# Kernel tuning notes

Measured on AMD Instinct MI355X. Metric: run time of the kernel, lower is better.

Reference implementation:

```python
import jax, jax.numpy as jnp
import numpy as np
from jax import lax

B, CIN, COUT, H, W = 4, 256, 256, 64, 64
KH = KW = 3
STRIDE = PAD = DIL = 1
GROUPS = 1
K = KH * KW
HO = (H + 2 * PAD - DIL * (KH - 1) - 1) // STRIDE + 1
WO = (W + 2 * PAD - DIL * (KW - 1) - 1) // STRIDE + 1
DN = ('NCHW', 'OIHW', 'NCHW')


def _sep_conv(x, dw, pw):
    # Separable2d: depthwise kxk conv (stride/pad/dilation) then pointwise 1x1.
    y = lax.conv_general_dilated(x, dw, (STRIDE, STRIDE), [(PAD, PAD), (PAD, PAD)],
                                 rhs_dilation=(DIL, DIL), feature_group_count=x.shape[1],
                                 dimension_numbers=DN)
    return lax.conv_general_dilated(y, pw, (1, 1), 'VALID', dimension_numbers=DN)


def _deform_conv2d(x, offset, mask, weight, bias):
    Bb, Cin, Hh, Ww = x.shape
    O = weight.shape[0]
    G = offset.shape[1] // (2 * K)  # offset groups
    offs = offset.reshape(Bb, G, K, 2, HO, WO)
    dy, dx = offs[:, :, :, 0], offs[:, :, :, 1]  # [B,G,K,Ho,Wo]
    ki, kj = jnp.meshgrid(jnp.arange(KH), jnp.arange(KW), indexing='ij')
    base_y = (-PAD + ki.reshape(K, 1) * DIL + jnp.arange(HO)[None, :] * STRIDE).astype(x.dtype)  # [K,Ho]
    base_x = (-PAD + kj.reshape(K, 1) * DIL + jnp.arange(WO)[None, :] * STRIDE).astype(x.dtype)  # [K,Wo]
    py = base_y[None, None, :, :, None] + dy  # [B,G,K,Ho,Wo]
    px = base_x[None, None, :, None, :] + dx

    xg = x.reshape(Bb, G, Cin // G, Hh, Ww)

    def bilinear(img, py, px):
        # img [C,H,W], py/px [K,Ho,Wo]; zero-padding outside bounds.
        y0 = jnp.floor(py)
        x0 = jnp.floor(px)
        out = jnp.zeros((img.shape[0],) + py.shape, img.dtype)
        for a, (iy, wy) in enumerate((((y0), (y0 + 1 - py)), ((y0 + 1), (py - y0)))):
            for b, (ix, wx) in enumerate((((x0), (x0 + 1 - px)), ((x0 + 1), (px - x0)))):
                valid = (iy >= 0) & (iy < Hh) & (ix >= 0) & (ix < Ww)
                iyc = jnp.clip(iy, 0, Hh - 1).astype(jnp.int32)
                ixc = jnp.clip(ix, 0, Ww - 1).astype(jnp.int32)
                v = img[:, iyc, ixc]  # [C,K,Ho,Wo]
                out = out + v * (wy * wx * valid)[None]
        return out

    sampled = jax.vmap(jax.vmap(bilinear))(xg, py, px)  # [B,G,C/G,K,Ho,Wo]
    m = mask.reshape(Bb, G, K, HO, WO)
    sampled = sampled * m[:, :, None]

    cols = sampled.reshape(Bb, Cin, K, HO, WO).reshape(Bb, GROUPS, Cin // GROUPS, K, HO, WO)
    wr = weight.reshape(GROUPS, O // GROUPS, Cin // GROUPS, K)
    out = jnp.einsum('bgckhw,gock->bgohw', cols, wr).reshape(Bb, O, HO, WO)
    return out + bias[None, :, None, None]


def setup_inputs() -> dict:
    key = jax.random.key(0)
    ks = jax.random.split(key, 7)
    x = jax.random.normal(ks[0], (B, CIN, H, W), jnp.float32)
    weight = jax.random.normal(ks[1], (COUT, CIN // GROUPS, KH, KW), jnp.float32) / np.sqrt(CIN * K)
    bias = jax.random.normal(ks[2], (COUT,), jnp.float32) * 0.01
    off_dw = jax.random.normal(ks[3], (CIN, 1, KH, KW), jnp.float32) * 0.01
    off_pw = jax.random.normal(ks[4], (2 * K * GROUPS, CIN, 1, 1), jnp.float32) * 0.01
    mask_dw = jax.random.normal(ks[5], (CIN, 1, KH, KW), jnp.float32) * 0.01
    mask_pw = jax.random.normal(ks[6], (K * GROUPS, CIN, 1, 1), jnp.float32) * 0.01
    return dict(x=x, weight=weight, bias=bias, off_dw=off_dw, off_pw=off_pw,
                mask_dw=mask_dw, mask_pw=mask_pw)


def reference(x, weight, bias, off_dw, off_pw, mask_dw, mask_pw):
    offset = _sep_conv(x, off_dw, off_pw)                       # [B,2*K,Ho,Wo]
    mask = jax.nn.sigmoid(_sep_conv(x, mask_dw, mask_pw)) * 2.0  # MaskSigmoid(scale=2)
    return _deform_conv2d(x, offset, mask, weight, bias)
```

## Files before the change

### kernel.cpp

```cpp
#include <hip/hip_runtime.h>

#define CIN   256
#define COUT  256
#define HH    64
#define WW    64
#define KD    2304
#define NPIX  16384
#define SPLIT 16
#define CPS   (CIN / SPLIT)

typedef __attribute__((ext_vector_type(8))) short  short8v;
typedef __attribute__((ext_vector_type(4))) float  float4v;
typedef __attribute__((ext_vector_type(4))) unsigned short ushort4v;
typedef __attribute__((ext_vector_type(2))) unsigned int uint2v;
typedef unsigned int u32;
typedef unsigned short u16;

__device__ __forceinline__ u16 f2bf(float f) {
  union { float f; unsigned u; } v; v.f = f;
  unsigned r = v.u + 0x7FFFu + ((v.u >> 16) & 1u);
  return (u16)(r >> 16);
}
__device__ __forceinline__ float bf2f(u16 h) {
  union { unsigned u; float f; } v; v.u = ((unsigned)h) << 16;
  return v.f;
}

__device__ __forceinline__ void gload_lds16(const void* g, void* l) {
  __builtin_amdgcn_global_load_lds((const __attribute__((address_space(1))) u32*)g,
                                   (__attribute__((address_space(3))) u32*)l, 16, 0, 0);
}

__global__ __launch_bounds__(256) void offmask_part_kernel(
    const float* __restrict__ x,
    const float* __restrict__ off_dw, const float* __restrict__ off_pw,
    const float* __restrict__ mask_dw, const float* __restrict__ mask_pw,
    float* __restrict__ part)
{
  int m = blockIdx.x * 256 + threadIdx.x;
  int s = blockIdx.y;
  int b = m >> 12, pix = m & 4095;
  int ho = pix >> 6, wo = pix & 63;
  const float* xb = x + (size_t)b * CIN * 4096;

  float acc[27];
#pragma unroll
  for (int j = 0; j < 27; ++j) acc[j] = 0.f;

  int c0 = s * CPS;
  for (int ci = 0; ci < CPS; ++ci) {
    int c = c0 + ci;
    const float* xc = xb + (size_t)c * 4096;
    float d_off = 0.f, d_msk = 0.f;
#pragma unroll
    for (int t = 0; t < 9; ++t) {
      int gy = ho + t / 3 - 1, gx = wo + t % 3 - 1;
      bool ok = (gy >= 0) & (gy < HH) & (gx >= 0) & (gx < WW);
      float v = ok ? xc[gy * 64 + gx] : 0.f;
      d_off += v * off_dw[c * 9 + t];
      d_msk += v * mask_dw[c * 9 + t];
    }
#pragma unroll
    for (int j = 0; j < 18; ++j) acc[j] += d_off * off_pw[j * 256 + c];
#pragma unroll
    for (int j = 0; j < 9; ++j) acc[18 + j] += d_msk * mask_pw[j * 256 + c];
  }
  float* pp = part + ((size_t)s * NPIX + m) * 32;
#pragma unroll
  for (int j = 0; j < 27; ++j) pp[j] = acc[j];
}

__global__ __launch_bounds__(256) void offmask_reduce_kernel(
    const float* __restrict__ part, float* __restrict__ rec)
{
  int i = blockIdx.x * 256 + threadIdx.x;
  int m = i >> 5, j = i & 31;
  if (j >= 27) { rec[i] = 0.f; return; }
  float sum = 0.f;
#pragma unroll
  for (int s = 0; s < SPLIT; ++s) sum += part[((size_t)s * NPIX + m) * 32 + j];
  rec[i] = (j < 18) ? sum : 2.f / (1.f + __expf(-sum));
}

__global__ __launch_bounds__(256) void wconv_kernel(const float* __restrict__ w,
                                                    u16* __restrict__ wb)
{
  int i = blockIdx.x * 256 + threadIdx.x;
  int co = i / KD, rem = i - co * KD;
  int c = rem / 9, kk = rem - c * 9;
  wb[co * KD + kk * 256 + c] = f2bf(w[i]);
}

__global__ __launch_bounds__(256) void xpose_kernel(const float* __restrict__ x,
                                                    u16* __restrict__ xt)
{
  __shared__ float t[64][65];
  int ptile = blockIdx.x;
  int ctile = blockIdx.y;
  int b     = blockIdx.z;
  int tid = threadIdx.x;
  const float* xb = x + (size_t)b * CIN * 4096 + (size_t)ctile * 64 * 4096 + ptile * 64;
#pragma unroll
  for (int i = 0; i < 16; ++i) {
    int c = i * 4 + (tid >> 6), p = tid & 63;
    t[c][p] = xb[(size_t)c * 4096 + p];
  }
  __syncthreads();
  u16* xo = xt + ((size_t)b * 4096 + ptile * 64) * 256 + ctile * 64;
#pragma unroll
  for (int i = 0; i < 16; ++i) {
    int p = i * 4 + (tid >> 6), c = tid & 63;
    xo[(size_t)p * 256 + c] = f2bf(t[c][p]);
  }
}

__global__ __launch_bounds__(512) void gemm_fused_kernel(
    const u16* __restrict__ A,
    const u16* __restrict__ xt,
    const float* __restrict__ rec,
    const float* __restrict__ bias,
    float* __restrict__ out,
    float* __restrict__ tmp)
{
  __shared__ __align__(16) u16 lA[2][256 * 32];
  __shared__ __align__(16) u16 lB[2][64 * 32];
  const int tid = threadIdx.x;
  const int bid = blockIdx.x;
  const int h   = bid & 1;
  const int ptile = bid >> 1;
  const int m0  = ptile * 64;
  const int b_img = ptile >> 6;
  const int cbase = h * 128;
  const int wave = tid >> 6, lane = tid & 63;
  const int wm = wave >> 1, wn = wave & 1;
  const int rl = lane & 15, kq = lane >> 4;
  const int sA = (kq ^ (rl & 3) ^ ((rl >> 2) & 3)) * 8;

  const int rA  = tid >> 2;
  const int koA = ((tid & 3) ^ (rA & 3) ^ ((rA >> 2) & 3)) * 8;
  const u16* aRow0 = A + (size_t)rA * KD + koA;
  const u16* aRow1 = A + (size_t)(rA + 128) * KD + koA;

  const int spx = tid >> 3;
  const int sc4 = (tid & 7) * 4;
  const int m_px = m0 + spx;
  const int ho = (m_px & 4095) >> 6, wo = m_px & 63;
  const float* rp = rec + (size_t)m_px * 32;
  const u16* xb = xt + (size_t)b_img * 4096 * 256;
  const int wAddr = spx * 32 +
                    ((((tid >> 1) & 3) ^ ((spx & 3) ^ ((spx >> 2) & 3))) * 8) +
                    (tid & 1) * 4;

  u32 cOff[4];
  float cW[4];

#define KCOL(t_) (((t_) >> 2) * 256 + cbase + ((t_) & 3) * 32)

#define CALC_CORNERS(kk_) do {                                             \
    float dy = rp[(kk_) * 2], dx = rp[(kk_) * 2 + 1], msk = rp[18 + (kk_)];\
    float py  = (float)(ho - 1 + ((kk_) / 3)) + dy;                        \
    float pxf = (float)(wo - 1 + ((kk_) % 3)) + dx;                        \
    float fy = floorf(py), fx = floorf(pxf);                               \
    int y0 = (int)fy, x0 = (int)fx;                                        \
    float wy1 = py - fy, wy0 = 1.f - wy1;                                  \
    float wx1 = pxf - fx, wx0 = 1.f - wx1;                                 \
    _Pragma("unroll")                                                      \
    for (int cr = 0; cr < 4; ++cr) {                                       \
      int iy = y0 + (cr >> 1), ix = x0 + (cr & 1);                         \
      bool valid = (iy >= 0) & (iy < HH) & (ix >= 0) & (ix < WW);          \
      int iyc = min(max(iy, 0), HH - 1), ixc = min(max(ix, 0), WW - 1);    \
      cOff[cr] = (u32)(iyc * 64 + ixc) * 256;                              \
      float wy = (cr >> 1) ? wy1 : wy0;                                    \
      float wx = (cr & 1) ? wx1 : wx0;                                     \
      cW[cr] = valid ? (wy * wx * msk) : 0.f;                              \
    }                                                                      \
  } while (0)

#define STAGE_A(t, bufi) do {                                              \
    int k0_ = KCOL(t);                                                     \
    gload_lds16(aRow0 + k0_, lA[bufi] + tid * 8);                          \
    gload_lds16(aRow1 + k0_, lA[bufi] + (tid + 512) * 8);                  \
  } while (0)

  float4v acc[4][2];
#pragma unroll
  for (int m = 0; m < 4; ++m)
#pragma unroll
    for (int n = 0; n < 2; ++n) acc[m][n] = float4v{0.f, 0.f, 0.f, 0.f};

  {
    CALC_CORNERS(0);
    int c0n = cbase + sc4;
    ushort4v v0 = *(const ushort4v*)(xb + cOff[0] + c0n);
    ushort4v v1 = *(const ushort4v*)(xb + cOff[1] + c0n);
    ushort4v v2 = *(const ushort4v*)(xb + cOff[2] + c0n);
    ushort4v v3 = *(const ushort4v*)(xb + cOff[3] + c0n);
    float a0 = cW[0]*bf2f(v0[0]) + cW[1]*bf2f(v1[0]) + cW[2]*bf2f(v2[0]) + cW[3]*bf2f(v3[0]);
    float a1 = cW[0]*bf2f(v0[1]) + cW[1]*bf2f(v1[1]) + cW[2]*bf2f(v2[1]) + cW[3]*bf2f(v3[1]);
    float a2 = cW[0]*bf2f(v0[2]) + cW[1]*bf2f(v1[2]) + cW[2]*bf2f(v2[2]) + cW[3]*bf2f(v3[2]);
    float a3 = cW[0]*bf2f(v0[3]) + cW[1]*bf2f(v1[3]) + cW[2]*bf2f(v2[3]) + cW[3]*bf2f(v3[3]);
    uint2v wv;
    wv[0] = (u32)f2bf(a0) | ((u32)f2bf(a1) << 16);
    wv[1] = (u32)f2bf(a2) | ((u32)f2bf(a3) << 16);
    *(uint2v*)&lB[0][wAddr] = wv;
    STAGE_A(0, 0);
  }
  __syncthreads();

#pragma unroll 4
  for (int ks = 0; ks < 36; ++ks) {
    const int cur = ks & 1;
    ushort4v v0, v1, v2, v3;
    const bool have = (ks < 35);
    if (have) {
      STAGE_A(ks + 1, cur ^ 1);
      int ksn = ks + 1;
      if ((ksn & 3) == 0) CALC_CORNERS(ksn >> 2);
      int c0n = cbase + (ksn & 3) * 32 + sc4;
      v0 = *(const ushort4v*)(xb + cOff[0] + c0n);
      v1 = *(const ushort4v*)(xb + cOff[1] + c0n);
      v2 = *(const ushort4v*)(xb + cOff[2] + c0n);
      v3 = *(const ushort4v*)(xb + cOff[3] + c0n);
    }
    short8v af[4], bf[2];
#pragma unroll
    for (int m = 0; m < 4; ++m)
      af[m] = *(const short8v*)&lA[cur][(wm * 64 + m * 16 + rl) * 32 + sA];
#pragma unroll
    for (int n = 0; n < 2; ++n)
      bf[n] = *(const short8v*)&lB[cur][(wn * 32 + n * 16 + rl) * 32 + sA];
#pragma unroll
    for (int m = 0; m < 4; ++m)
#pragma unroll
      for (int n = 0; n < 2; ++n)
        acc[m][n] = __builtin_amdgcn_mfma_f32_16x16x32_bf16(af[m], bf[n], acc[m][n], 0, 0, 0);
    if (have) {
      float a0 = cW[0]*bf2f(v0[0]) + cW[1]*bf2f(v1[0]) + cW[2]*bf2f(v2[0]) + cW[3]*bf2f(v3[0]);
      float a1 = cW[0]*bf2f(v0[1]) + cW[1]*bf2f(v1[1]) + cW[2]*bf2f(v2[1]) + cW[3]*bf2f(v3[1]);
      float a2 = cW[0]*bf2f(v0[2]) + cW[1]*bf2f(v1[2]) + cW[2]*bf2f(v2[2]) + cW[3]*bf2f(v3[2]);
      float a3 = cW[0]*bf2f(v0[3]) + cW[1]*bf2f(v1[3]) + cW[2]*bf2f(v2[3]) + cW[3]*bf2f(v3[3]);
      uint2v wv;
      wv[0] = (u32)f2bf(a0) | ((u32)f2bf(a1) << 16);
      wv[1] = (u32)f2bf(a2) | ((u32)f2bf(a3) << 16);
      *(uint2v*)&lB[cur ^ 1][wAddr] = wv;
    }
    __syncthreads();
  }
#undef STAGE_A
#undef CALC_CORNERS
#undef KCOL

  const int p_base = (m0 & 4095) + wn * 32;
  float* db = (h ? tmp : out) + (size_t)b_img * COUT * 4096;
#pragma unroll
  for (int m = 0; m < 4; ++m) {
#pragma unroll
    for (int j = 0; j < 4; ++j) {
      int co = wm * 64 + m * 16 + kq * 4 + j;
      float bv = h ? 0.f : bias[co];
#pragma unroll
      for (int n = 0; n < 2; ++n) {
        int pp = p_base + n * 16 + rl;
        db[(size_t)co * 4096 + pp] = acc[m][n][j] + bv;
      }
    }
  }
}

__global__ __launch_bounds__(256) void add_kernel(float* __restrict__ out,
                                                  const float* __restrict__ tmp)
{
  int i = blockIdx.x * 256 + threadIdx.x;
  float4v a = *(const float4v*)(out + (size_t)i * 4);
  float4v b = *(const float4v*)(tmp + (size_t)i * 4);
  a += b;
  *(float4v*)(out + (size_t)i * 4) = a;
}

extern "C" void kernel_launch(void* const* d_in, const int* in_sizes, int n_in,
                              void* d_out, int out_size, void* d_ws, size_t ws_size,
                              hipStream_t stream) {
  const float* x       = (const float*)d_in[0];
  const float* weight  = (const float*)d_in[1];
  const float* bias    = (const float*)d_in[2];
  const float* off_dw  = (const float*)d_in[3];
  const float* off_pw  = (const float*)d_in[4];
  const float* mask_dw = (const float*)d_in[5];
  const float* mask_pw = (const float*)d_in[6];

  if (ws_size < 45219840ull) return;
  float* rec  = (float*)d_ws;
  u16*   wb   = (u16*)((char*)d_ws + 2097152);
  u16*   xt   = (u16*)((char*)d_ws + 3276800);
  float* part = (float*)((char*)d_ws + 11665408);
  float* tmp  = part;
  float* out  = (float*)d_out;

  wconv_kernel<<<dim3(2304), dim3(256), 0, stream>>>(weight, wb);
  offmask_part_kernel<<<dim3(NPIX / 256, SPLIT), dim3(256), 0, stream>>>(
      x, off_dw, off_pw, mask_dw, mask_pw, part);
  offmask_reduce_kernel<<<dim3(NPIX * 32 / 256), dim3(256), 0, stream>>>(part, rec);
  xpose_kernel<<<dim3(64, 4, 4), dim3(256), 0, stream>>>(x, xt);
  gemm_fused_kernel<<<dim3(512), dim3(512), 0, stream>>>(wb, xt, rec, bias, out, tmp);
  add_kernel<<<dim3((COUT * NPIX / 4) / 256), dim3(256), 0, stream>>>(out, tmp);
}
```

Measured before the change: 106.5 us.

## Switch to fp16 packed bilinear blend and split-K into four channel quarters

Weights and transposed activations are now stored as fp16 instead of bf16. The bilinear blend uses packed half2 multiply-adds, and the GEMM uses the f16 MFMA instead of the bf16 one. The GEMM grid doubles from 512 to 1024 blocks by splitting the channel reduction into four 64-channel quarters, which should improve occupancy across CUs and shorten each block's K loop. The cost is three partial output buffers plus a heavier final add kernel that reads them, and fp16 overflow and precision risk in the blend and inputs.

Result: slower. 110.8 us (+4.0%).

```diff
diff --git a/kernel.cpp b/kernel.cpp
--- a/kernel.cpp
+++ b/kernel.cpp
@@ -11,20 +11,15 @@
 
 typedef __attribute__((ext_vector_type(8))) short  short8v;
 typedef __attribute__((ext_vector_type(4))) float  float4v;
-typedef __attribute__((ext_vector_type(4))) unsigned short ushort4v;
 typedef __attribute__((ext_vector_type(2))) unsigned int uint2v;
+typedef _Float16 h2 __attribute__((ext_vector_type(2)));
+typedef _Float16 h8 __attribute__((ext_vector_type(8)));
 typedef unsigned int u32;
 typedef unsigned short u16;
 
-__device__ __forceinline__ u16 f2bf(float f) {
-  union { float f; unsigned u; } v; v.f = f;
-  unsigned r = v.u + 0x7FFFu + ((v.u >> 16) & 1u);
-  return (u16)(r >> 16);
-}
-__device__ __forceinline__ float bf2f(u16 h) {
-  union { unsigned u; float f; } v; v.u = ((unsigned)h) << 16;
-  return v.f;
-}
+__device__ __forceinline__ h2 as_h2(u32 v) { union { u32 u; h2 h; } x; x.u = v; return x.h; }
+__device__ __forceinline__ u32 as_u32(h2 h) { union { u32 u; h2 h; } x; x.h = h; return x.u; }
+__device__ __forceinline__ u16 f2h_bits(float f) { _Float16 h = (_Float16)f; return *(u16*)&h; }
 
 __device__ __forceinline__ void gload_lds16(const void* g, void* l) {
   __builtin_amdgcn_global_load_lds((const __attribute__((address_space(1))) u32*)g,
@@ -88,7 +83,7 @@
   int i = blockIdx.x * 256 + threadIdx.x;
   int co = i / KD, rem = i - co * KD;
   int c = rem / 9, kk = rem - c * 9;
-  wb[co * KD + kk * 256 + c] = f2bf(w[i]);
+  wb[co * KD + kk * 256 + c] = f2h_bits(w[i]);
 }
 
 __global__ __launch_bounds__(256) void xpose_kernel(const float* __restrict__ x,
@@ -110,7 +105,7 @@
 #pragma unroll
   for (int i = 0; i < 16; ++i) {
     int p = i * 4 + (tid >> 6), c = tid & 63;
-    xo[(size_t)p * 256 + c] = f2bf(t[c][p]);
+    xo[(size_t)p * 256 + c] = f2h_bits(t[c][p]);
   }
 }
 
@@ -126,11 +121,11 @@
   __shared__ __align__(16) u16 lB[2][64 * 32];
   const int tid = threadIdx.x;
   const int bid = blockIdx.x;
-  const int h   = bid & 1;
-  const int ptile = bid >> 1;
+  const int h   = bid & 3;
+  const int ptile = bid >> 2;
   const int m0  = ptile * 64;
   const int b_img = ptile >> 6;
-  const int cbase = h * 128;
+  const int cbase = h * 64;
   const int wave = tid >> 6, lane = tid & 63;
   const int wm = wave >> 1, wn = wave & 1;
   const int rl = lane & 15, kq = lane >> 4;
@@ -152,9 +147,9 @@
                     (tid & 1) * 4;
 
   u32 cOff[4];
-  float cW[4];
-
-#define KCOL(t_) (((t_) >> 2) * 256 + cbase + ((t_) & 3) * 32)
+  h2  wh[4];
+
+#define KCOL(t_) (((t_) >> 1) * 256 + cbase + ((t_) & 1) * 32)
 
 #define CALC_CORNERS(kk_) do {                                             \
     float dy = rp[(kk_) * 2], dx = rp[(kk_) * 2 + 1], msk = rp[18 + (kk_)];\
@@ -172,7 +167,9 @@
       cOff[cr] = (u32)(iyc * 64 + ixc) * 256;                              \
       float wy = (cr >> 1) ? wy1 : wy0;                                    \
       float wx = (cr & 1) ? wx1 : wx0;                                     \
-      cW[cr] = valid ? (wy * wx * msk) : 0.f;                              \
+      float wf = valid ? (wy * wx * msk) : 0.f;                            \
+      _Float16 hw = (_Float16)wf;                                          \
+      wh[cr] = (h2){hw, hw};                                               \
     }                                                                      \
   } while (0)
 
@@ -182,6 +179,15 @@
     gload_lds16(aRow1 + k0_, lA[bufi] + (tid + 512) * 8);                  \
   } while (0)
 
+#define BLEND_WRITE(bufi, v0_, v1_, v2_, v3_) do {                         \
+    h2 a01 = wh[0] * as_h2((v0_)[0]) + wh[1] * as_h2((v1_)[0]);            \
+    a01   += wh[2] * as_h2((v2_)[0]) + wh[3] * as_h2((v3_)[0]);            \
+    h2 a23 = wh[0] * as_h2((v0_)[1]) + wh[1] * as_h2((v1_)[1]);            \
+    a23   += wh[2] * as_h2((v2_)[1]) + wh[3] * as_h2((v3_)[1]);            \
+    uint2v wv; wv[0] = as_u32(a01); wv[1] = as_u32(a23);                   \
+    *(uint2v*)&lB[bufi][wAddr] = wv;                                       \
+  } while (0)
+
   float4v acc[4][2];
 #pragma unroll
   for (int m = 0; m < 4; ++m)
@@ -191,67 +197,53 @@
   {
     CALC_CORNERS(0);
     int c0n = cbase + sc4;
-    ushort4v v0 = *(const ushort4v*)(xb + cOff[0] + c0n);
-    ushort4v v1 = *(const ushort4v*)(xb + cOff[1] + c0n);
-    ushort4v v2 = *(const ushort4v*)(xb + cOff[2] + c0n);
-    ushort4v v3 = *(const ushort4v*)(xb + cOff[3] + c0n);
-    float a0 = cW[0]*bf2f(v0[0]) + cW[1]*bf2f(v1[0]) + cW[2]*bf2f(v2[0]) + cW[3]*bf2f(v3[0]);
-    float a1 = cW[0]*bf2f(v0[1]) + cW[1]*bf2f(v1[1]) + cW[2]*bf2f(v2[1]) + cW[3]*bf2f(v3[1]);
-    float a2 = cW[0]*bf2f(v0[2]) + cW[1]*bf2f(v1[2]) + cW[2]*bf2f(v2[2]) + cW[3]*bf2f(v3[2]);
-    float a3 = cW[0]*bf2f(v0[3]) + cW[1]*bf2f(v1[3]) + cW[2]*bf2f(v2[3]) + cW[3]*bf2f(v3[3]);
-    uint2v wv;
-    wv[0] = (u32)f2bf(a0) | ((u32)f2bf(a1) << 16);
-    wv[1] = (u32)f2bf(a2) | ((u32)f2bf(a3) << 16);
-    *(uint2v*)&lB[0][wAddr] = wv;
+    uint2v v0 = *(const uint2v*)(xb + cOff[0] + c0n);
+    uint2v v1 = *(const uint2v*)(xb + cOff[1] + c0n);
+    uint2v v2 = *(const uint2v*)(xb + cOff[2] + c0n);
+    uint2v v3 = *(const uint2v*)(xb + cOff[3] + c0n);
+    BLEND_WRITE(0, v0, v1, v2, v3);
     STAGE_A(0, 0);
   }
   __syncthreads();
 
-#pragma unroll 4
-  for (int ks = 0; ks < 36; ++ks) {
+#pragma unroll 2
+  for (int ks = 0; ks < 18; ++ks) {
     const int cur = ks & 1;
-    ushort4v v0, v1, v2, v3;
-    const bool have = (ks < 35);
+    uint2v v0, v1, v2, v3;
+    const bool have = (ks < 17);
     if (have) {
       STAGE_A(ks + 1, cur ^ 1);
       int ksn = ks + 1;
-      if ((ksn & 3) == 0) CALC_CORNERS(ksn >> 2);
-      int c0n = cbase + (ksn & 3) * 32 + sc4;
-      v0 = *(const ushort4v*)(xb + cOff[0] + c0n);
-      v1 = *(const ushort4v*)(xb + cOff[1] + c0n);
-      v2 = *(const ushort4v*)(xb + cOff[2] + c0n);
-      v3 = *(const ushort4v*)(xb + cOff[3] + c0n);
+      if ((ksn & 1) == 0) CALC_CORNERS(ksn >> 1);
+      int c0n = cbase + (ksn & 1) * 32 + sc4;
+      v0 = *(const uint2v*)(xb + cOff[0] + c0n);
+      v1 = *(const uint2v*)(xb + cOff[1] + c0n);
+      v2 = *(const uint2v*)(xb + cOff[2] + c0n);
+      v3 = *(const uint2v*)(xb + cOff[3] + c0n);
     }
-    short8v af[4], bf[2];
+    h8 af[4], bf[2];
 #pragma unroll
     for (int m = 0; m < 4; ++m)
-      af[m] = *(const short8v*)&lA[cur][(wm * 64 + m * 16 + rl) * 32 + sA];
+      af[m] = *(const h8*)&lA[cur][(wm * 64 + m * 16 + rl) * 32 + sA];
 #pragma unroll
     for (int n = 0; n < 2; ++n)
-      bf[n] = *(const short8v*)&lB[cur][(wn * 32 + n * 16 + rl) * 32 + sA];
+      bf[n] = *(const h8*)&lB[cur][(wn * 32 + n * 16 + rl) * 32 + sA];
 #pragma unroll
     for (int m = 0; m < 4; ++m)
 #pragma unroll
       for (int n = 0; n < 2; ++n)
-        acc[m][n] = __builtin_amdgcn_mfma_f32_16x16x32_bf16(af[m], bf[n], acc[m][n], 0, 0, 0);
-    if (have) {
-      float a0 = cW[0]*bf2f(v0[0]) + cW[1]*bf2f(v1[0]) + cW[2]*bf2f(v2[0]) + cW[3]*bf2f(v3[0]);
-      float a1 = cW[0]*bf2f(v0[1]) + cW[1]*bf2f(v1[1]) + cW[2]*bf2f(v2[1]) + cW[3]*bf2f(v3[1]);
-      float a2 = cW[0]*bf2f(v0[2]) + cW[1]*bf2f(v1[2]) + cW[2]*bf2f(v2[2]) + cW[3]*bf2f(v3[2]);
-      float a3 = cW[0]*bf2f(v0[3]) + cW[1]*bf2f(v1[3]) + cW[2]*bf2f(v2[3]) + cW[3]*bf2f(v3[3]);
-      uint2v wv;
-      wv[0] = (u32)f2bf(a0) | ((u32)f2bf(a1) << 16);
-      wv[1] = (u32)f2bf(a2) | ((u32)f2bf(a3) << 16);
-      *(uint2v*)&lB[cur ^ 1][wAddr] = wv;
-    }
+        acc[m][n] = __builtin_amdgcn_mfma_f32_16x16x32_f16(af[m], bf[n], acc[m][n], 0, 0, 0);
+    if (have) BLEND_WRITE(cur ^ 1, v0, v1, v2, v3);
     __syncthreads();
   }
 #undef STAGE_A
 #undef CALC_CORNERS
+#undef BLEND_WRITE
 #undef KCOL
 
   const int p_base = (m0 & 4095) + wn * 32;
-  float* db = (h ? tmp : out) + (size_t)b_img * COUT * 4096;
+  float* db = (h ? (tmp + (size_t)(h - 1) * COUT * NPIX) : out) +
+              (size_t)b_img * COUT * 4096;
 #pragma unroll
   for (int m = 0; m < 4; ++m) {
 #pragma unroll
@@ -270,11 +262,13 @@
 __global__ __launch_bounds__(256) void add_kernel(float* __restrict__ out,
                                                   const float* __restrict__ tmp)
 {
-  int i = blockIdx.x * 256 + threadIdx.x;
-  float4v a = *(const float4v*)(out + (size_t)i * 4);
-  float4v b = *(const float4v*)(tmp + (size_t)i * 4);
-  a += b;
-  *(float4v*)(out + (size_t)i * 4) = a;
+  size_t i = ((size_t)blockIdx.x * 256 + threadIdx.x) * 4;
+  float4v a  = *(const float4v*)(out + i);
+  float4v b0 = *(const float4v*)(tmp + i);
+  float4v b1 = *(const float4v*)(tmp + (size_t)COUT * NPIX + i);
+  float4v b2 = *(const float4v*)(tmp + (size_t)2 * COUT * NPIX + i);
+  a += b0 + b1 + b2;
+  *(float4v*)(out + i) = a;
 }
 
 extern "C" void kernel_launch(void* const* d_in, const int* in_sizes, int n_in,
@@ -288,7 +282,7 @@
   const float* mask_dw = (const float*)d_in[5];
   const float* mask_pw = (const float*)d_in[6];
 
-  if (ws_size < 45219840ull) return;
+  if (ws_size < 61997056ull) return;
   float* rec  = (float*)d_ws;
   u16*   wb   = (u16*)((char*)d_ws + 2097152);
   u16*   xt   = (u16*)((char*)d_ws + 3276800);
@@ -301,6 +295,6 @@
       x, off_dw, off_pw, mask_dw, mask_pw, part);
   offmask_reduce_kernel<<<dim3(NPIX * 32 / 256), dim3(256), 0, stream>>>(part, rec);
   xpose_kernel<<<dim3(64, 4, 4), dim3(256), 0, stream>>>(x, xt);
-  gemm_fused_kernel<<<dim3(512), dim3(512), 0, stream>>>(wb, xt, rec, bias, out, tmp);
-  add_kernel<<<dim3((COUT * NPIX / 4) / 256), dim3(256), 0, stream>>>(out, tmp);
-}
+  gemm_fused_kernel<<<dim3(1024), dim3(512), 0, stream>>>(wb, xt, rec, bias, out, tmp);
+  add_kernel<<<dim3(COUT * NPIX / 4 / 256), dim3(256), 0, stream>>>(out, tmp);
+}
```
